# Kernel tuning notes

Hardware: AMD Instinct MI355X
Metric: run time of the kernel (lower is better)

The kernel has to match this reference:

```python
import jax, jax.numpy as jnp
import numpy as np

REP_THR = 0.6
BORDER = 10


def setup_inputs() -> dict:
    key = jax.random.key(0)
    repeatability = jax.random.uniform(key, (8, 1, 2048, 2048), dtype=jnp.float32)
    return {"repeatability": repeatability}


def reference(repeatability):
    # 3x3 max pool, stride 1, pad 1 (torch pads with -inf for max pool)
    local_max = jax.lax.reduce_window(
        repeatability,
        -jnp.inf,
        jax.lax.max,
        window_dimensions=(1, 1, 3, 3),
        window_strides=(1, 1, 1, 1),
        padding=[(0, 0), (0, 0), (1, 1), (1, 1)],
    )
    maxima = (repeatability == local_max) & (repeatability >= REP_THR)
    # border mask: zero out a 10-pixel frame
    B, C, H, W = repeatability.shape
    border = jnp.zeros((H, W), dtype=bool).at[BORDER:-BORDER, BORDER:-BORDER].set(True)
    maxima = maxima & border  # broadcast over (B, C)
    # Original returns maxima.nonzero().t()[2:4] (data-dependent shape);
    # for jit-compatibility we return the dense boolean mask as float32 —
    # the (y, x) indices are exactly the nonzero positions of this mask.
    return maxima.astype(jnp.float32)
```

## Files before the change

### kernel.cpp

```cpp
#include <hip/hip_runtime.h>
#include <math.h>

#define IMG_H 2048
#define IMG_W 2048
#define NB    8
#define BORDER 10
#define REP_THR 0.6f

__global__ __launch_bounds__(256) void nms_kernel(const float* __restrict__ in,
                                                  float* __restrict__ out) {
    const int tid = blockIdx.x * blockDim.x + threadIdx.x;
    const int x4 = (tid & 511) << 2;
    const int y  = (tid >> 9) & (IMG_H - 1);
    const int b  = tid >> 20;

    const size_t img_off = (size_t)b * IMG_H * IMG_W;
    float* o = out + img_off + (size_t)y * IMG_W + x4;

    if (y < BORDER || y >= IMG_H - BORDER || x4 == 0 || x4 == IMG_W - 4) {
        *(float4*)o = make_float4(0.f, 0.f, 0.f, 0.f);
        return;
    }

    const float* rm = in + img_off + (size_t)(y - 1) * IMG_W + x4;
    const float* rc = in + img_off + (size_t)y       * IMG_W + x4;
    const float* rp = in + img_off + (size_t)(y + 1) * IMG_W + x4;

    const float4 cm = *(const float4*)rm;
    const float4 cc = *(const float4*)rc;
    const float4 cp = *(const float4*)rp;

    const float lm = rm[-1], qm = rm[4];
    const float lc = rc[-1], qc = rc[4];
    const float lp = rp[-1], qp = rp[4];

    const float hm0 = fmaxf(lm,   fmaxf(cm.x, cm.y));
    const float hm1 = fmaxf(cm.x, fmaxf(cm.y, cm.z));
    const float hm2 = fmaxf(cm.y, fmaxf(cm.z, cm.w));
    const float hm3 = fmaxf(cm.z, fmaxf(cm.w, qm));

    const float hc0 = fmaxf(lc,   fmaxf(cc.x, cc.y));
    const float hc1 = fmaxf(cc.x, fmaxf(cc.y, cc.z));
    const float hc2 = fmaxf(cc.y, fmaxf(cc.z, cc.w));
    const float hc3 = fmaxf(cc.z, fmaxf(cc.w, qc));

    const float hp0 = fmaxf(lp,   fmaxf(cp.x, cp.y));
    const float hp1 = fmaxf(cp.x, fmaxf(cp.y, cp.z));
    const float hp2 = fmaxf(cp.y, fmaxf(cp.z, cp.w));
    const float hp3 = fmaxf(cp.z, fmaxf(cp.w, qp));

    const float m0 = fmaxf(hm0, fmaxf(hc0, hp0));
    const float m1 = fmaxf(hm1, fmaxf(hc1, hp1));
    const float m2 = fmaxf(hm2, fmaxf(hc2, hp2));
    const float m3 = fmaxf(hm3, fmaxf(hc3, hp3));

    const bool bx0 = (x4 + 0 >= BORDER) && (x4 + 0 < IMG_W - BORDER);
    const bool bx1 = (x4 + 1 >= BORDER) && (x4 + 1 < IMG_W - BORDER);
    const bool bx2 = (x4 + 2 >= BORDER) && (x4 + 2 < IMG_W - BORDER);
    const bool bx3 = (x4 + 3 >= BORDER) && (x4 + 3 < IMG_W - BORDER);

    float4 r;
    r.x = (cc.x == m0 && cc.x >= REP_THR && bx0) ? 1.f : 0.f;
    r.y = (cc.y == m1 && cc.y >= REP_THR && bx1) ? 1.f : 0.f;
    r.z = (cc.z == m2 && cc.z >= REP_THR && bx2) ? 1.f : 0.f;
    r.w = (cc.w == m3 && cc.w >= REP_THR && bx3) ? 1.f : 0.f;

    *(float4*)o = r;
}

extern "C" void kernel_launch(void* const* d_in, const int* in_sizes, int n_in,
                              void* d_out, int out_size, void* d_ws, size_t ws_size,
                              hipStream_t stream) {
    const float* in = (const float*)d_in[0];
    float* out = (float*)d_out;
    const int total_threads = NB * IMG_H * (IMG_W / 4);
    const int block = 256;
    const int grid = total_threads / block;
    nms_kernel<<<grid, block, 0, stream>>>(in, out);
}
```

Before: 230.8 us.

## Process 4x4 tile per thread to reuse vertical stencil rows

```diff
diff --git a/kernel.cpp b/kernel.cpp
--- a/kernel.cpp
+++ b/kernel.cpp
@@ -10,62 +10,68 @@
 __global__ __launch_bounds__(256) void nms_kernel(const float* __restrict__ in,
                                                   float* __restrict__ out) {
     const int tid = blockIdx.x * blockDim.x + threadIdx.x;
-    const int x4 = (tid & 511) << 2;
-    const int y  = (tid >> 9) & (IMG_H - 1);
-    const int b  = tid >> 20;
+    const int gx = tid & 511;
+    const int gy = (tid >> 9) & 511;
+    const int b  = tid >> 18;
+
+    const int x4 = gx << 2;
+    const int y0 = gy << 2;
 
     const size_t img_off = (size_t)b * IMG_H * IMG_W;
-    float* o = out + img_off + (size_t)y * IMG_W + x4;
+    float* obase = out + img_off + (size_t)y0 * IMG_W + x4;
 
-    if (y < BORDER || y >= IMG_H - BORDER || x4 == 0 || x4 == IMG_W - 4) {
-        *(float4*)o = make_float4(0.f, 0.f, 0.f, 0.f);
+    if (y0 + 4 <= BORDER || y0 >= IMG_H - BORDER || gx == 0 || gx == 511) {
+        const float4 z = make_float4(0.f, 0.f, 0.f, 0.f);
+        *(float4*)(obase + 0 * IMG_W) = z;
+        *(float4*)(obase + 1 * IMG_W) = z;
+        *(float4*)(obase + 2 * IMG_W) = z;
+        *(float4*)(obase + 3 * IMG_W) = z;
         return;
     }
 
-    const float* rm = in + img_off + (size_t)(y - 1) * IMG_W + x4;
-    const float* rc = in + img_off + (size_t)y       * IMG_W + x4;
-    const float* rp = in + img_off + (size_t)(y + 1) * IMG_W + x4;
+    const float* base = in + img_off + (size_t)(y0 - 1) * IMG_W + x4;
 
-    const float4 cm = *(const float4*)rm;
-    const float4 cc = *(const float4*)rc;
-    const float4 cp = *(const float4*)rp;
-
-    const float lm = rm[-1], qm = rm[4];
-    const float lc = rc[-1], qc = rc[4];
-    const float lp = rp[-1], qp = rp[4];
-
-    const float hm0 = fmaxf(lm,   fmaxf(cm.x, cm.y));
-    const float hm1 = fmaxf(cm.x, fmaxf(cm.y, cm.z));
-    const float hm2 = fmaxf(cm.y, fmaxf(cm.z, cm.w));
-    const float hm3 = fmaxf(cm.z, fmaxf(cm.w, qm));
-
-    const float hc0 = fmaxf(lc,   fmaxf(cc.x, cc.y));
-    const float hc1 = fmaxf(cc.x, fmaxf(cc.y, cc.z));
-    const float hc2 = fmaxf(cc.y, fmaxf(cc.z, cc.w));
-    const float hc3 = fmaxf(cc.z, fmaxf(cc.w, qc));
-
-    const float hp0 = fmaxf(lp,   fmaxf(cp.x, cp.y));
-    const float hp1 = fmaxf(cp.x, fmaxf(cp.y, cp.z));
-    const float hp2 = fmaxf(cp.y, fmaxf(cp.z, cp.w));
-    const float hp3 = fmaxf(cp.z, fmaxf(cp.w, qp));
-
-    const float m0 = fmaxf(hm0, fmaxf(hc0, hp0));
-    const float m1 = fmaxf(hm1, fmaxf(hc1, hp1));
-    const float m2 = fmaxf(hm2, fmaxf(hc2, hp2));
-    const float m3 = fmaxf(hm3, fmaxf(hc3, hp3));
+    float4 h[6];
+    float4 c[4];
+#pragma unroll
+    for (int r = 0; r < 6; ++r) {
+        const float* row = base + (size_t)r * IMG_W;
+        const float4 v = *(const float4*)row;
+        const float  l = row[-1];
+        const float  q = row[4];
+        float4 hh;
+        hh.x = fmaxf(l,   fmaxf(v.x, v.y));
+        hh.y = fmaxf(v.x, fmaxf(v.y, v.z));
+        hh.z = fmaxf(v.y, fmaxf(v.z, v.w));
+        hh.w = fmaxf(v.z, fmaxf(v.w, q));
+        h[r] = hh;
+        if (r >= 1 && r <= 4) c[r - 1] = v;
+    }
 
     const bool bx0 = (x4 + 0 >= BORDER) && (x4 + 0 < IMG_W - BORDER);
     const bool bx1 = (x4 + 1 >= BORDER) && (x4 + 1 < IMG_W - BORDER);
     const bool bx2 = (x4 + 2 >= BORDER) && (x4 + 2 < IMG_W - BORDER);
     const bool bx3 = (x4 + 3 >= BORDER) && (x4 + 3 < IMG_W - BORDER);
 
-    float4 r;
-    r.x = (cc.x == m0 && cc.x >= REP_THR && bx0) ? 1.f : 0.f;
-    r.y = (cc.y == m1 && cc.y >= REP_THR && bx1) ? 1.f : 0.f;
-    r.z = (cc.z == m2 && cc.z >= REP_THR && bx2) ? 1.f : 0.f;
-    r.w = (cc.w == m3 && cc.w >= REP_THR && bx3) ? 1.f : 0.f;
+#pragma unroll
+    for (int j = 0; j < 4; ++j) {
+        const int y = y0 + j;
+        const bool rowok = (y >= BORDER) && (y < IMG_H - BORDER);
 
-    *(float4*)o = r;
+        float4 m;
+        m.x = fmaxf(h[j].x, fmaxf(h[j + 1].x, h[j + 2].x));
+        m.y = fmaxf(h[j].y, fmaxf(h[j + 1].y, h[j + 2].y));
+        m.z = fmaxf(h[j].z, fmaxf(h[j + 1].z, h[j + 2].z));
+        m.w = fmaxf(h[j].w, fmaxf(h[j + 1].w, h[j + 2].w));
+
+        float4 r;
+        r.x = (c[j].x == m.x && c[j].x >= REP_THR && bx0 && rowok) ? 1.f : 0.f;
+        r.y = (c[j].y == m.y && c[j].y >= REP_THR && bx1 && rowok) ? 1.f : 0.f;
+        r.z = (c[j].z == m.z && c[j].z >= REP_THR && bx2 && rowok) ? 1.f : 0.f;
+        r.w = (c[j].w == m.w && c[j].w >= REP_THR && bx3 && rowok) ? 1.f : 0.f;
+
+        *(float4*)(obase + (size_t)j * IMG_W) = r;
+    }
 }
 
 extern "C" void kernel_launch(void* const* d_in, const int* in_sizes, int n_in,
@@ -73,7 +79,7 @@
                               hipStream_t stream) {
     const float* in = (const float*)d_in[0];
     float* out = (float*)d_out;
-    const int total_threads = NB * IMG_H * (IMG_W / 4);
+    const int total_threads = NB * (IMG_H / 4) * (IMG_W / 4);
     const int block = 256;
     const int grid = total_threads / block;
     nms_kernel<<<grid, block, 0, stream>>>(in, out);
```

Measured after the change: 226.5 us. About the same (-1.8%).
